# Kernel optimization log

Hardware: AMD Instinct MI355X
Metric: run time of the kernel (lower is better)

## Reference

```python
import jax, jax.numpy as jnp
import numpy as np

D = 1024        # number of Hawkes dimensions (N_g * K)
M = 32768       # number of events
BETA = 1.0      # fixed exponential-kernel decay
T_MAX = 1000    # observation horizon
EPS_MU = 1e-06
EPS_LOG = 1e-08


def setup_inputs() -> dict:
    key = jax.random.key(0)
    k1, k2, k3, k4 = jax.random.split(key, 4)
    t_events = jnp.sort(jax.random.uniform(k1, (M,), dtype=jnp.float32) * T_MAX)
    marks = jax.random.randint(k2, (M,), 0, D)
    # learned params around the torch init (-3 / -4) with a little noise
    log_mu = jnp.full((D,), -3.0, dtype=jnp.float32) + 0.1 * jax.random.normal(k3, (D,), dtype=jnp.float32)
    log_alpha = jnp.full((D, D), -4.0, dtype=jnp.float32) + 0.1 * jax.random.normal(k4, (D, D), dtype=jnp.float32)
    return {"t_events": t_events, "marks": marks, "log_mu": log_mu,
            "log_alpha": log_alpha, "T_max": T_MAX}


def reference(t_events, marks, log_mu, log_alpha, T_max):
    """Hawkes log-likelihood; faithful translation of XuHawkesTorch.intensity_loglik."""
    mu = jax.nn.softplus(log_mu) + EPS_MU          # [D]
    alpha = jax.nn.softplus(log_alpha)             # [D, D]
    T_max = jnp.asarray(T_max, dtype=t_events.dtype)

    # inter-event gaps; dt[0] = 0 so first event sees no decay (matches torch loop)
    dt = jnp.diff(t_events, prepend=t_events[:1])  # [M]
    decay = jnp.exp(-BETA * dt)                    # [M]

    def step(S, inp):
        dec, d = inp
        S = dec * S                                # exp-decay of excitation state
        lam_d = mu[d] + alpha[d] @ S               # intensity at event d
        ll = jnp.log(lam_d + EPS_LOG)
        S = S.at[d].add(1.0)                       # event adds unit excitation
        return S, ll

    S0 = jnp.zeros((D,), dtype=t_events.dtype)
    _, lls = jax.lax.scan(step, S0, (decay, marks))

    # compensator integral over [0, T_max]
    one_minus_exp = 1.0 - jnp.exp(-BETA * (T_max - t_events))   # [M]
    contrib = jax.ops.segment_sum(one_minus_exp, marks, num_segments=D)  # [D]
    integral = mu * T_max + alpha @ (contrib / BETA)            # [D]

    return lls.sum() - integral.sum()
```

## Files before the change

kernel.cpp:

```cpp
#include <hip/hip_runtime.h>


#define D 1024
#define M 32768
#define C 64
#define NC (M / C)
#define NB (NC * 8)
#define NG 16
#define GC (NC / NG)
#define TMAXV 1000.0f
#define EPSMU 1e-6f
#define EPSLOG 1e-8f

__device__ __forceinline__ float softplus(float x) {
    return (x > 0.0f) ? (x + log1pf(__expf(-x))) : log1pf(__expf(x));
}

__device__ __forceinline__ unsigned short f2bf(float x) {
    unsigned u = __float_as_uint(x);
    return (unsigned short)((u + 0x7FFFu + ((u >> 16) & 1u)) >> 16);
}
__device__ __forceinline__ float bf2f(unsigned short h) {
    return __uint_as_float(((unsigned)h) << 16);
}

__global__ void k1(const float* __restrict__ t_ev, const int* __restrict__ marks,
                   const float* __restrict__ log_alpha, const float* __restrict__ log_mu,
                   unsigned short* __restrict__ ab, float* __restrict__ mu,
                   float* __restrict__ P, float* __restrict__ Sl, float* __restrict__ A) {
    __shared__ float Lh[GC * 256];
    __shared__ float dec[GC];
    __shared__ float tns[GC];
    int t = threadIdx.x;
    int b = blockIdx.x;

    if (b < 256) {
        int r0 = b * 4;
        float4 cs = {0.f, 0.f, 0.f, 0.f};
        for (int r = 0; r < 4; ++r) {
            const float4* src = (const float4*)(log_alpha + (size_t)(r0 + r) * D);
            float4 v = src[t];
            float4 a;
            a.x = softplus(v.x);
            a.y = softplus(v.y);
            a.z = softplus(v.z);
            a.w = softplus(v.w);
            cs.x += a.x; cs.y += a.y; cs.z += a.z; cs.w += a.w;
            ushort4 h;
            h.x = f2bf(a.x); h.y = f2bf(a.y); h.z = f2bf(a.z); h.w = f2bf(a.w);
            ((ushort4*)(ab + (size_t)(r0 + r) * D))[t] = h;
        }
        ((float4*)(P + (size_t)b * D))[t] = cs;
    } else if (b == 256) {
#pragma unroll
        for (int q = 0; q < 4; ++q) {
            int k = t + 256 * q;
            mu[k] = softplus(log_mu[k]) + EPSMU;
        }
    } else {
        int fb = b - 257;
        int g = fb >> 2, db = fb & 3;
#pragma unroll
        for (int q = 0; q < GC; ++q) Lh[q * 256 + t] = 0.0f;
        if (t < GC) {
            int gc = g * GC + t;
            float tn = (gc + 1 < NC) ? t_ev[(gc + 1) * C] : t_ev[M - 1];
            tns[t] = tn;
            dec[t] = (gc + 1 < NC) ? __expf(t_ev[gc * C] - tn) : 1.0f;
        }
        __syncthreads();
        int base = g * (GC * C);
#pragma unroll
        for (int it = 0; it < 8; ++it) {
            int e = it * 256 + t;
            float te = t_ev[base + e];
            int m = marks[base + e];
            int lc = e >> 6;
            int ml = m - db * 256;
            if ((unsigned)ml < 256u) atomicAdd(&Lh[lc * 256 + ml], __expf(te - tns[lc]));
        }
        __syncthreads();
        int k = db * 256 + t;
        float S = 0.0f;
        for (int lc = 0; lc < GC; ++lc) {
            Sl[(size_t)(g * GC + lc) * D + k] = S;
            S = S * dec[lc] + Lh[lc * 256 + t];
        }
        A[(size_t)g * D + k] = S;
    }
}

__global__ void k_mid(const float* __restrict__ P, float* __restrict__ colsum,
                      const float* __restrict__ t_ev, const float* __restrict__ A,
                      float* __restrict__ Sg, float* __restrict__ cumdec) {
    int t = threadIdx.x;
    if (blockIdx.x < 8) {
        __shared__ float red[8][128];
        int colL = t & 127, seg = t >> 7;
        int col = blockIdx.x * 128 + colL;
        float s = 0.0f;
#pragma unroll
        for (int j = 0; j < 32; ++j)
            s += P[(size_t)(seg * 32 + j) * D + col];
        red[seg][colL] = s;
        __syncthreads();
        if (t < 128) {
            float v = 0.0f;
#pragma unroll
            for (int k = 0; k < 8; ++k) v += red[k][t];
            colsum[blockIdx.x * 128 + t] = v;
        }
    } else {
        __shared__ float dec[NC];
        __shared__ float Pg[NG];
        if (t < NC)
            dec[t] = (t + 1 < NC) ? __expf(t_ev[t * C] - t_ev[(t + 1) * C]) : 1.0f;
        __syncthreads();
        if (t < NC) {
            int g = t >> 5, r = t & 31;
            float p = 1.0f;
            for (int j = 0; j < r; ++j) p *= dec[g * GC + j];
            cumdec[t] = p;
            if (r == GC - 1) Pg[g] = p * dec[t];
        }
        __syncthreads();
        float a[NG];
#pragma unroll
        for (int g2 = 0; g2 < NG; ++g2) a[g2] = A[(size_t)g2 * D + t];
        float S = 0.0f;
#pragma unroll
        for (int g2 = 0; g2 < NG; ++g2) {
            Sg[(size_t)g2 * D + t] = S;
            S = S * Pg[g2] + a[g2];
        }
    }
}

__launch_bounds__(256)
__global__ void k_main(const float* __restrict__ t_ev, const int* __restrict__ marks,
                       const unsigned short* __restrict__ ab, const float* __restrict__ mu,
                       const float* __restrict__ colsum, const float* __restrict__ Sl,
                       const float* __restrict__ Sg, const float* __restrict__ cumdec,
                       float* __restrict__ llp, float* __restrict__ compp) {
    __shared__ float S_lds[D];
    __shared__ float t_lds[C];
    __shared__ int d_lds[C];
    __shared__ float red[8];
    int t = threadIdx.x;
    int c = blockIdx.x >> 3, sub = blockIdx.x & 7;
    int g = c >> 5;
    float cd = cumdec[c];
#pragma unroll
    for (int q = 0; q < 4; ++q) {
        int k = t + 256 * q;
        S_lds[k] = Sl[(size_t)c * D + k] + Sg[(size_t)g * D + k] * cd;
    }
    if (t < C) {
        t_lds[t] = t_ev[c * C + t];
        d_lds[t] = marks[c * C + t];
    }
    __syncthreads();
    int wave = t >> 6, lane = t & 63;
    float t0 = t_lds[0];
    float ll_acc = 0.0f, comp_acc = 0.0f;
#pragma unroll
    for (int i = sub * 8 + wave; i < sub * 8 + 8; i += 4) {
        int row = d_lds[i];
        float ti = t_lds[i];
        float mu_r = mu[row];
        float cs_r = colsum[row];
        const uint4* arow = (const uint4*)(ab + (size_t)row * D);
        float acc_dot = 0.0f;
#pragma unroll
        for (int u = 0; u < 2; ++u) {
            uint4 pk = arow[2 * lane + u];
            const float4* sp = (const float4*)(S_lds + 16 * lane + 8 * u);
            float4 s0 = sp[0], s1 = sp[1];
            acc_dot += __uint_as_float(pk.x << 16) * s0.x
                     + __uint_as_float(pk.x & 0xFFFF0000u) * s0.y
                     + __uint_as_float(pk.y << 16) * s0.z
                     + __uint_as_float(pk.y & 0xFFFF0000u) * s0.w
                     + __uint_as_float(pk.z << 16) * s1.x
                     + __uint_as_float(pk.z & 0xFFFF0000u) * s1.y
                     + __uint_as_float(pk.w << 16) * s1.z
                     + __uint_as_float(pk.w & 0xFFFF0000u) * s1.w;
        }
        float part = acc_dot * __expf(t0 - ti);
        if (lane < i) {
            part += bf2f(ab[(size_t)row * D + d_lds[lane]]) * __expf(t_lds[lane] - ti);
        }
#pragma unroll
        for (int off = 32; off > 0; off >>= 1) part += __shfl_xor(part, off);
        if (lane == 0) {
            ll_acc += __logf(mu_r + part + EPSLOG);
            comp_acc += cs_r * (1.0f - __expf(ti - TMAXV));
        }
    }
    if (lane == 0) {
        red[wave] = ll_acc;
        red[4 + wave] = comp_acc;
    }
    __syncthreads();
    if (t == 0) {
        llp[blockIdx.x] = red[0] + red[1] + red[2] + red[3];
        compp[blockIdx.x] = red[4] + red[5] + red[6] + red[7];
    }
}

__global__ void k_final(const float* __restrict__ llp, const float* __restrict__ compp,
                        const float* __restrict__ mu, float* __restrict__ out) {
    __shared__ float r_ll[1024], r_cm[1024], r_mu[1024];
    int t = threadIdx.x;
    float sll = 0.0f, scm = 0.0f;
#pragma unroll
    for (int j = 0; j < 4; ++j) {
        sll += llp[t + 1024 * j];
        scm += compp[t + 1024 * j];
    }
    r_ll[t] = sll;
    r_cm[t] = scm;
    r_mu[t] = mu[t];
    __syncthreads();
    for (int off = 512; off > 0; off >>= 1) {
        if (t < off) {
            r_ll[t] += r_ll[t + off];
            r_cm[t] += r_cm[t + off];
            r_mu[t] += r_mu[t + off];
        }
        __syncthreads();
    }
    if (t == 0) out[0] = r_ll[0] - (TMAXV * r_mu[0] + r_cm[0]);
}

extern "C" void kernel_launch(void* const* d_in, const int* in_sizes, int n_in,
                              void* d_out, int out_size, void* d_ws, size_t ws_size,
                              hipStream_t stream) {
    const float* t_ev = (const float*)d_in[0];
    const int* marks = (const int*)d_in[1];
    const float* log_mu = (const float*)d_in[2];
    const float* log_alpha = (const float*)d_in[3];
    float* out = (float*)d_out;

    float* w = (float*)d_ws;
    unsigned short* ab = (unsigned short*)w;
    float* Sl = w + (size_t)D * D / 2;
    float* mu = Sl + (size_t)NC * D;
    float* colsum = mu + D;
    float* P = colsum + D;
    float* llp = P + (size_t)256 * D;
    float* compp = llp + NB;
    float* A = compp + NB;
    float* Sg = A + (size_t)NG * D;
    float* cumdec = Sg + (size_t)NG * D;

    k1<<<321, 256, 0, stream>>>(t_ev, marks, log_alpha, log_mu, ab, mu, P, Sl, A);
    k_mid<<<9, 1024, 0, stream>>>(P, colsum, t_ev, A, Sg, cumdec);
    k_main<<<NB, 256, 0, stream>>>(t_ev, marks, ab, mu, colsum, Sl, Sg, cumdec, llp, compp);
    k_final<<<1, 1024, 0, stream>>>(llp, compp, mu, out);
}
```

Before: 90.11 us.

## Compute compensator via segment-summed contrib in k1/k_mid and drop per-event compensator work

The compensator term moves out of the main event kernel. k1 accumulates per-mark (1-exp(t-T)) sums in shared memory, and k_mid dots the alpha column sums with them. The serial cumulative-decay loop in k_mid is replaced by a direct exp of the time difference, now computed inline in k_main. This shortens the k_mid critical path and removes the colsum load and compensator arithmetic from k_main, at the cost of extra shared atomics in k1 and a small extra reduction in k_mid.

Result: no change. 91.10 us (+1.1%).

```diff
diff --git a/kernel.cpp b/kernel.cpp
--- a/kernel.cpp
+++ b/kernel.cpp
@@ -27,8 +27,10 @@
 __global__ void k1(const float* __restrict__ t_ev, const int* __restrict__ marks,
                    const float* __restrict__ log_alpha, const float* __restrict__ log_mu,
                    unsigned short* __restrict__ ab, float* __restrict__ mu,
-                   float* __restrict__ P, float* __restrict__ Sl, float* __restrict__ A) {
+                   float* __restrict__ P, float* __restrict__ Sl, float* __restrict__ A,
+                   float* __restrict__ contrib_p) {
     __shared__ float Lh[GC * 256];
+    __shared__ float Ch[256];
     __shared__ float dec[GC];
     __shared__ float tns[GC];
     int t = threadIdx.x;
@@ -62,6 +64,7 @@
         int g = fb >> 2, db = fb & 3;
 #pragma unroll
         for (int q = 0; q < GC; ++q) Lh[q * 256 + t] = 0.0f;
+        Ch[t] = 0.0f;
         if (t < GC) {
             int gc = g * GC + t;
             float tn = (gc + 1 < NC) ? t_ev[(gc + 1) * C] : t_ev[M - 1];
@@ -77,10 +80,14 @@
             int m = marks[base + e];
             int lc = e >> 6;
             int ml = m - db * 256;
-            if ((unsigned)ml < 256u) atomicAdd(&Lh[lc * 256 + ml], __expf(te - tns[lc]));
+            if ((unsigned)ml < 256u) {
+                atomicAdd(&Lh[lc * 256 + ml], __expf(te - tns[lc]));
+                atomicAdd(&Ch[ml], 1.0f - __expf(te - TMAXV));
+            }
         }
         __syncthreads();
         int k = db * 256 + t;
+        contrib_p[(size_t)g * D + k] = Ch[t];
         float S = 0.0f;
         for (int lc = 0; lc < GC; ++lc) {
             Sl[(size_t)(g * GC + lc) * D + k] = S;
@@ -90,12 +97,13 @@
     }
 }
 
-__global__ void k_mid(const float* __restrict__ P, float* __restrict__ colsum,
+__global__ void k_mid(const float* __restrict__ P, const float* __restrict__ contrib_p,
                       const float* __restrict__ t_ev, const float* __restrict__ A,
-                      float* __restrict__ Sg, float* __restrict__ cumdec) {
+                      float* __restrict__ Sg, float* __restrict__ comp_p) {
     int t = threadIdx.x;
     if (blockIdx.x < 8) {
         __shared__ float red[8][128];
+        __shared__ float pr[128];
         int colL = t & 127, seg = t >> 7;
         int col = blockIdx.x * 128 + colL;
         float s = 0.0f;
@@ -108,20 +116,23 @@
             float v = 0.0f;
 #pragma unroll
             for (int k = 0; k < 8; ++k) v += red[k][t];
-            colsum[blockIdx.x * 128 + t] = v;
-        }
+            float cs = 0.0f;
+#pragma unroll
+            for (int g = 0; g < NG; ++g) cs += contrib_p[(size_t)g * D + col];
+            pr[t] = v * cs;
+        }
+        __syncthreads();
+        for (int off = 64; off > 0; off >>= 1) {
+            if (t < off) pr[t] += pr[t + off];
+            __syncthreads();
+        }
+        if (t == 0) comp_p[blockIdx.x] = pr[0];
     } else {
-        __shared__ float dec[NC];
         __shared__ float Pg[NG];
-        if (t < NC)
-            dec[t] = (t + 1 < NC) ? __expf(t_ev[t * C] - t_ev[(t + 1) * C]) : 1.0f;
-        __syncthreads();
-        if (t < NC) {
-            int g = t >> 5, r = t & 31;
-            float p = 1.0f;
-            for (int j = 0; j < r; ++j) p *= dec[g * GC + j];
-            cumdec[t] = p;
-            if (r == GC - 1) Pg[g] = p * dec[t];
+        if (t < NG) {
+            float Tg = t_ev[t * (GC * C)];
+            float Tn = (t < NG - 1) ? t_ev[(t + 1) * (GC * C)] : t_ev[M - 1];
+            Pg[t] = __expf(Tg - Tn);
         }
         __syncthreads();
         float a[NG];
@@ -139,17 +150,16 @@
 __launch_bounds__(256)
 __global__ void k_main(const float* __restrict__ t_ev, const int* __restrict__ marks,
                        const unsigned short* __restrict__ ab, const float* __restrict__ mu,
-                       const float* __restrict__ colsum, const float* __restrict__ Sl,
-                       const float* __restrict__ Sg, const float* __restrict__ cumdec,
-                       float* __restrict__ llp, float* __restrict__ compp) {
+                       const float* __restrict__ Sl, const float* __restrict__ Sg,
+                       float* __restrict__ llp) {
     __shared__ float S_lds[D];
     __shared__ float t_lds[C];
     __shared__ int d_lds[C];
-    __shared__ float red[8];
+    __shared__ float red[4];
     int t = threadIdx.x;
     int c = blockIdx.x >> 3, sub = blockIdx.x & 7;
     int g = c >> 5;
-    float cd = cumdec[c];
+    float cd = __expf(t_ev[(size_t)g * (GC * C)] - t_ev[(size_t)c * C]);
 #pragma unroll
     for (int q = 0; q < 4; ++q) {
         int k = t + 256 * q;
@@ -162,13 +172,12 @@
     __syncthreads();
     int wave = t >> 6, lane = t & 63;
     float t0 = t_lds[0];
-    float ll_acc = 0.0f, comp_acc = 0.0f;
+    float ll_acc = 0.0f;
 #pragma unroll
     for (int i = sub * 8 + wave; i < sub * 8 + 8; i += 4) {
         int row = d_lds[i];
         float ti = t_lds[i];
         float mu_r = mu[row];
-        float cs_r = colsum[row];
         const uint4* arow = (const uint4*)(ab + (size_t)row * D);
         float acc_dot = 0.0f;
 #pragma unroll
@@ -191,34 +200,22 @@
         }
 #pragma unroll
         for (int off = 32; off > 0; off >>= 1) part += __shfl_xor(part, off);
-        if (lane == 0) {
-            ll_acc += __logf(mu_r + part + EPSLOG);
-            comp_acc += cs_r * (1.0f - __expf(ti - TMAXV));
-        }
-    }
-    if (lane == 0) {
-        red[wave] = ll_acc;
-        red[4 + wave] = comp_acc;
-    }
+        if (lane == 0) ll_acc += __logf(mu_r + part + EPSLOG);
+    }
+    if (lane == 0) red[wave] = ll_acc;
     __syncthreads();
-    if (t == 0) {
-        llp[blockIdx.x] = red[0] + red[1] + red[2] + red[3];
-        compp[blockIdx.x] = red[4] + red[5] + red[6] + red[7];
-    }
-}
-
-__global__ void k_final(const float* __restrict__ llp, const float* __restrict__ compp,
+    if (t == 0) llp[blockIdx.x] = red[0] + red[1] + red[2] + red[3];
+}
+
+__global__ void k_final(const float* __restrict__ llp, const float* __restrict__ comp_p,
                         const float* __restrict__ mu, float* __restrict__ out) {
     __shared__ float r_ll[1024], r_cm[1024], r_mu[1024];
     int t = threadIdx.x;
-    float sll = 0.0f, scm = 0.0f;
-#pragma unroll
-    for (int j = 0; j < 4; ++j) {
-        sll += llp[t + 1024 * j];
-        scm += compp[t + 1024 * j];
-    }
+    float sll = 0.0f;
+#pragma unroll
+    for (int j = 0; j < 4; ++j) sll += llp[t + 1024 * j];
     r_ll[t] = sll;
-    r_cm[t] = scm;
+    r_cm[t] = (t < 8) ? comp_p[t] : 0.0f;
     r_mu[t] = mu[t];
     __syncthreads();
     for (int off = 512; off > 0; off >>= 1) {
@@ -245,16 +242,15 @@
     unsigned short* ab = (unsigned short*)w;
     float* Sl = w + (size_t)D * D / 2;
     float* mu = Sl + (size_t)NC * D;
-    float* colsum = mu + D;
-    float* P = colsum + D;
-    float* llp = P + (size_t)256 * D;
-    float* compp = llp + NB;
-    float* A = compp + NB;
+    float* P = mu + D;
+    float* contrib_p = P + (size_t)256 * D;
+    float* comp_p = contrib_p + (size_t)NG * D;
+    float* llp = comp_p + 8;
+    float* A = llp + NB;
     float* Sg = A + (size_t)NG * D;
-    float* cumdec = Sg + (size_t)NG * D;
-
-    k1<<<321, 256, 0, stream>>>(t_ev, marks, log_alpha, log_mu, ab, mu, P, Sl, A);
-    k_mid<<<9, 1024, 0, stream>>>(P, colsum, t_ev, A, Sg, cumdec);
-    k_main<<<NB, 256, 0, stream>>>(t_ev, marks, ab, mu, colsum, Sl, Sg, cumdec, llp, compp);
-    k_final<<<1, 1024, 0, stream>>>(llp, compp, mu, out);
-}
+
+    k1<<<321, 256, 0, stream>>>(t_ev, marks, log_alpha, log_mu, ab, mu, P, Sl, A, contrib_p);
+    k_mid<<<9, 1024, 0, stream>>>(P, contrib_p, t_ev, A, Sg, comp_p);
+    k_main<<<NB, 256, 0, stream>>>(t_ev, marks, ab, mu, Sl, Sg, llp);
+    k_final<<<1, 1024, 0, stream>>>(llp, comp_p, mu, out);
+}
```
